# Performance work log

Hardware: AMD Instinct MI355X
Metric: run time of the kernel (lower is better)

The kernel has to match this reference:

```python
import jax, jax.numpy as jnp
import numpy as np

B, S, H, NH = 4, 2048, 1024, 16
HS = H // NH  # head size 64


def setup_inputs() -> dict:
    key = jax.random.key(0)
    ks = jax.random.split(key, 12)
    inv = 1.0 / np.sqrt(H)
    d = {
        "query": jax.random.normal(ks[0], (B, S, H), jnp.float32),
        "key": jax.random.normal(ks[1], (B, S, H), jnp.float32),
        "value": jax.random.normal(ks[2], (B, S, H), jnp.float32),
        "causal_mask": jnp.tril(jnp.ones((S, S), dtype=bool)),
        "Wq": jax.random.uniform(ks[3], (H, H), jnp.float32, -inv, inv),
        "bq": jax.random.uniform(ks[4], (H,), jnp.float32, -inv, inv),
        "Wk": jax.random.uniform(ks[5], (H, H), jnp.float32, -inv, inv),
        "bk": jax.random.uniform(ks[6], (H,), jnp.float32, -inv, inv),
        "Wv": jax.random.uniform(ks[7], (H, H), jnp.float32, -inv, inv),
        "bv": jax.random.uniform(ks[8], (H,), jnp.float32, -inv, inv),
        "Wo": jax.random.uniform(ks[9], (H, H), jnp.float32, -inv, inv),
        "bo": jax.random.uniform(ks[10], (H,), jnp.float32, -inv, inv),
    }
    return d


def reference(query, key, value, causal_mask, Wq, bq, Wk, bk, Wv, bv, Wo, bo):
    # Linear projections (torch Linear: x @ W.T + b)
    q = query @ Wq.T + bq
    k = key @ Wk.T + bk
    v = value @ Wv.T + bv
    # [B, NH, S, HS]
    q = q.reshape(B, S, NH, HS).transpose(0, 2, 1, 3)
    k = k.reshape(B, S, NH, HS).transpose(0, 2, 1, 3)
    v = v.reshape(B, S, NH, HS).transpose(0, 2, 1, 3)
    scores = jnp.einsum("bhqd,bhkd->bhqk", q, k) / jnp.sqrt(jnp.float32(HS))
    scores = jnp.where(causal_mask[None, None, :, :], scores, -jnp.inf)
    attn = jax.nn.softmax(scores, axis=-1)
    ctx = jnp.einsum("bhqk,bhkd->bhqd", attn, v)
    ctx = ctx.transpose(0, 2, 1, 3).reshape(B, S, H)
    return ctx @ Wo.T + bo
```

## Files before the change

### kernel.cpp

```cpp
#include <hip/hip_runtime.h>
#include <hip/hip_bf16.h>
#include <math.h>

#define B_  4
#define S_  2048
#define H_  1024
#define NH_ 16
#define HS_ 64

typedef __attribute__((ext_vector_type(8))) short bf16x8;
typedef __attribute__((ext_vector_type(4))) float f32x4;

__device__ __forceinline__ short f2bf(float f) {
    unsigned u = __builtin_bit_cast(unsigned, f);
    u += 0x7FFFu + ((u >> 16) & 1u);
    return (short)(u >> 16);
}

typedef __attribute__((address_space(3))) void lds_void;
typedef const __attribute__((address_space(1))) void g_void;
__device__ __forceinline__ void gl_lds16(const void* g, void* l) {
    __builtin_amdgcn_global_load_lds((g_void*)g, (lds_void*)l, 16, 0, 0);
}

__global__ __launch_bounds__(256) void cvt_all_k(
    const float* __restrict__ a0, const float* __restrict__ a1,
    const float* __restrict__ a2, const float* __restrict__ w0,
    const float* __restrict__ w1, const float* __restrict__ w2,
    const float* __restrict__ w3,
    short* o0, short* o1, short* o2, short* o3, short* o4, short* o5, short* o6)
{
    const int y = blockIdx.y;
    const float* ins[7]  = {a0, a1, a2, w0, w1, w2, w3};
    short*       outs[7] = {o0, o1, o2, o3, o4, o5, o6};
    const int n8 = (y < 3) ? (int)((size_t)B_ * S_ * H_ / 8) : (int)((size_t)H_ * H_ / 8);
    const int i = blockIdx.x * 256 + threadIdx.x;
    if (i >= n8) return;
    const float4* p = (const float4*)ins[y] + (size_t)i * 2;
    float4 a = p[0], b = p[1];
    bf16x8 o;
    o[0] = f2bf(a.x); o[1] = f2bf(a.y); o[2] = f2bf(a.z); o[3] = f2bf(a.w);
    o[4] = f2bf(b.x); o[5] = f2bf(b.y); o[6] = f2bf(b.z); o[7] = f2bf(b.w);
    *(bf16x8*)(outs[y] + (size_t)i * 8) = o;
}

__device__ __forceinline__ void gemm_core(
    const short* __restrict__ A, const short* __restrict__ W,
    int m0, int n0, short* As, short* Ws, f32x4 acc[4][4])
{
    const int tid  = threadIdx.x;
    const int w    = tid >> 6;
    const int lane = tid & 63;
    const int l15  = lane & 15;
    const int q4   = lane >> 4;
    const int wm   = w >> 1;
    const int wn   = w & 1;
    const int K    = 1024;

    const char* Abase = (const char*)A + (size_t)m0 * K * 2;
    const char* Wbase = (const char*)W + (size_t)n0 * K * 2;

    #pragma unroll
    for (int mi = 0; mi < 4; ++mi)
        #pragma unroll
        for (int ni = 0; ni < 4; ++ni)
            acc[mi][ni] = (f32x4){0.f, 0.f, 0.f, 0.f};

    for (int k0 = 0; k0 < K; k0 += 32) {
        __syncthreads();
        #pragma unroll
        for (int t = 0; t < 2; ++t) {
            const int ob = t * 4096 + w * 1024;
            const int o  = ob + lane * 16;
            const int row = o >> 6;
            const int kb  = o & 63;
            gl_lds16(Abase + (size_t)row * (K * 2) + k0 * 2 + kb, (char*)As + ob);
            gl_lds16(Wbase + (size_t)row * (K * 2) + k0 * 2 + kb, (char*)Ws + ob);
        }
        __syncthreads();

        bf16x8 af[4], bf[4];
        #pragma unroll
        for (int mi = 0; mi < 4; ++mi)
            af[mi] = *(const bf16x8*)(As + (wm * 64 + mi * 16 + l15) * 32 + q4 * 8);
        #pragma unroll
        for (int ni = 0; ni < 4; ++ni)
            bf[ni] = *(const bf16x8*)(Ws + (wn * 64 + ni * 16 + l15) * 32 + q4 * 8);
        #pragma unroll
        for (int mi = 0; mi < 4; ++mi)
            #pragma unroll
            for (int ni = 0; ni < 4; ++ni)
                acc[mi][ni] = __builtin_amdgcn_mfma_f32_16x16x32_bf16(
                    af[mi], bf[ni], acc[mi][ni], 0, 0, 0);
    }
}

__global__ __launch_bounds__(256) void gemm_proj_k(
    const short* __restrict__ Aq, const short* __restrict__ Wqb,
    const float* __restrict__ bq, short* __restrict__ qb,
    const short* __restrict__ Ak, const short* __restrict__ Wkb,
    const float* __restrict__ bk, short* __restrict__ kb,
    const short* __restrict__ Wvb, const short* __restrict__ Av,
    const float* __restrict__ bv, short* __restrict__ vtb)
{
    __shared__ short As[128 * 32];
    __shared__ short Ws[128 * 32];

    const int z = blockIdx.z;
    const short *A, *W; const float* bias; short* out;
    if (z == 0)      { A = Aq;  W = Wqb; bias = bq; out = qb;  }
    else if (z == 1) { A = Ak;  W = Wkb; bias = bk; out = kb;  }
    else             { A = Wvb; W = Av;  bias = bv; out = vtb; }
    const int m0 = (z == 2 ? blockIdx.y : blockIdx.x) * 128;
    const int n0 = (z == 2 ? blockIdx.x : blockIdx.y) * 128;

    f32x4 acc[4][4];
    gemm_core(A, W, m0, n0, As, Ws, acc);

    const int tid  = threadIdx.x;
    const int w    = tid >> 6;
    const int lane = tid & 63;
    const int l15  = lane & 15;
    const int q4   = lane >> 4;
    const int wm   = w >> 1;
    const int wn   = w & 1;

    #pragma unroll
    for (int mi = 0; mi < 4; ++mi) {
        #pragma unroll
        for (int r = 0; r < 4; ++r) {
            const int m = m0 + wm * 64 + mi * 16 + q4 * 4 + r;
            #pragma unroll
            for (int ni = 0; ni < 4; ++ni) {
                const int n = n0 + wn * 64 + ni * 16 + l15;
                const float v = acc[mi][ni][r] + bias[z == 2 ? m : n];
                if (z != 2) {
                    const int b = m >> 11, s = m & (S_ - 1);
                    const int h = n >> 6,  d = n & (HS_ - 1);
                    out[(((size_t)b * NH_ + h) * S_ + s) * HS_ + d] = f2bf(v);
                } else {
                    const int b = n >> 11, s = n & (S_ - 1);
                    const int h = m >> 6,  d = m & (HS_ - 1);
                    out[(((size_t)b * NH_ + h) * HS_ + d) * S_ + s] = f2bf(v);
                }
            }
        }
    }
}

__global__ __launch_bounds__(256) void gemm_out_k(
    const short* __restrict__ A, const short* __restrict__ W,
    const float* __restrict__ bias, float* __restrict__ Cout)
{
    __shared__ short As[128 * 32];
    __shared__ short Ws[128 * 32];
    const int m0 = blockIdx.x * 128;
    const int n0 = blockIdx.y * 128;

    f32x4 acc[4][4];
    gemm_core(A, W, m0, n0, As, Ws, acc);

    const int tid  = threadIdx.x;
    const int w    = tid >> 6;
    const int lane = tid & 63;
    const int l15  = lane & 15;
    const int q4   = lane >> 4;
    const int wm   = w >> 1;
    const int wn   = w & 1;

    #pragma unroll
    for (int mi = 0; mi < 4; ++mi)
        #pragma unroll
        for (int r = 0; r < 4; ++r) {
            const int m = m0 + wm * 64 + mi * 16 + q4 * 4 + r;
            #pragma unroll
            for (int ni = 0; ni < 4; ++ni) {
                const int n = n0 + wn * 64 + ni * 16 + l15;
                Cout[(size_t)m * H_ + n] = acc[mi][ni][r] + bias[n];
            }
        }
}

#define PAD_ 72

__global__ __launch_bounds__(256) void attn_mfma(
    const short* __restrict__ Q, const short* __restrict__ K,
    const short* __restrict__ VT, short* __restrict__ O)
{
    __shared__ short Ks[64 * PAD_];
    __shared__ short Vt[64 * PAD_];
    __shared__ short Pl[4][32 * PAD_];

    const int tid  = threadIdx.x;
    const int w    = tid >> 6;
    const int lane = tid & 63;
    const int l15  = lane & 15;
    const int q4   = lane >> 4;
    const int bh   = blockIdx.y;
    const size_t base = (size_t)bh * S_ * HS_;
    const int b = bh >> 4;
    const int h = bh & 15;
    const float SC = 0.125f * 1.44269504f;

    #pragma unroll 1
    for (int pass = 0; pass < 2; ++pass) {
        const int qt = pass ? (15 - blockIdx.x) : blockIdx.x;

        bf16x8 aQ[2][2];
        #pragma unroll
        for (int mi = 0; mi < 2; ++mi) {
            const int qrow = qt * 128 + w * 32 + mi * 16 + l15;
            #pragma unroll
            for (int kh = 0; kh < 2; ++kh)
                aQ[mi][kh] = *(const bf16x8*)(Q + base + (size_t)qrow * HS_ + kh * 32 + q4 * 8);
        }

        f32x4 accO[2][4];
        float l_p[2][4];
        #pragma unroll
        for (int mi = 0; mi < 2; ++mi) {
            #pragma unroll
            for (int db = 0; db < 4; ++db) accO[mi][db] = (f32x4){0.f, 0.f, 0.f, 0.f};
            #pragma unroll
            for (int r = 0; r < 4; ++r) l_p[mi][r] = 0.f;
        }

        const int ktmax = 2 * qt + 1;
        for (int kt = 0; kt <= ktmax; ++kt) {
            __syncthreads();
            #pragma unroll
            for (int t = 0; t < 2; ++t) {
                const int c  = tid + t * 256;
                const int r  = c >> 3;
                const int e8 = (c & 7) * 8;
                *(bf16x8*)(&Ks[r * PAD_ + e8]) =
                    *(const bf16x8*)(K + base + (size_t)(kt * 64 + r) * HS_ + e8);
                *(bf16x8*)(&Vt[r * PAD_ + e8]) =
                    *(const bf16x8*)(VT + base + (size_t)r * S_ + kt * 64 + e8);
            }
            __syncthreads();

            f32x4 sb[2][4];
            #pragma unroll
            for (int nb = 0; nb < 4; ++nb) {
                const short* kr = &Ks[(nb * 16 + l15) * PAD_ + q4 * 8];
                bf16x8 b0 = *(const bf16x8*)(kr);
                bf16x8 b1 = *(const bf16x8*)(kr + 32);
                #pragma unroll
                for (int mi = 0; mi < 2; ++mi) {
                    f32x4 a = (f32x4){0.f, 0.f, 0.f, 0.f};
                    a = __builtin_amdgcn_mfma_f32_16x16x32_bf16(aQ[mi][0], b0, a, 0, 0, 0);
                    a = __builtin_amdgcn_mfma_f32_16x16x32_bf16(aQ[mi][1], b1, a, 0, 0, 0);
                    sb[mi][nb] = a;
                }
            }

            const bool need_mask = (kt >= 2 * qt);
            #pragma unroll
            for (int mi = 0; mi < 2; ++mi) {
                const int qb0 = qt * 128 + w * 32 + mi * 16 + q4 * 4;
                if (need_mask) {
                    #pragma unroll
                    for (int nb = 0; nb < 4; ++nb) {
                        const int kj = kt * 64 + nb * 16 + l15;
                        #pragma unroll
                        for (int r = 0; r < 4; ++r)
                            if (kj > qb0 + r) sb[mi][nb][r] = -INFINITY;
                    }
                }
                short* pw = &Pl[w][0];
                #pragma unroll
                for (int nb = 0; nb < 4; ++nb) {
                    #pragma unroll
                    for (int r = 0; r < 4; ++r) {
                        const float p = exp2f(sb[mi][nb][r] * SC);
                        l_p[mi][r] += p;
                        pw[(mi * 16 + q4 * 4 + r) * PAD_ + nb * 16 + l15] = f2bf(p);
                    }
                }
            }

            bf16x8 aP[2][2];
            #pragma unroll
            for (int mi = 0; mi < 2; ++mi)
                #pragma unroll
                for (int kh = 0; kh < 2; ++kh)
                    aP[mi][kh] = *(const bf16x8*)(&Pl[w][(mi * 16 + l15) * PAD_ + kh * 32 + q4 * 8]);
            #pragma unroll
            for (int db = 0; db < 4; ++db) {
                const short* vr = &Vt[(db * 16 + l15) * PAD_ + q4 * 8];
                bf16x8 b0 = *(const bf16x8*)(vr);
                bf16x8 b1 = *(const bf16x8*)(vr + 32);
                #pragma unroll
                for (int mi = 0; mi < 2; ++mi) {
                    accO[mi][db] = __builtin_amdgcn_mfma_f32_16x16x32_bf16(aP[mi][0], b0, accO[mi][db], 0, 0, 0);
                    accO[mi][db] = __builtin_amdgcn_mfma_f32_16x16x32_bf16(aP[mi][1], b1, accO[mi][db], 0, 0, 0);
                }
            }
        }

        #pragma unroll
        for (int mi = 0; mi < 2; ++mi) {
            #pragma unroll
            for (int r = 0; r < 4; ++r) {
                float ls = l_p[mi][r];
                ls += __shfl_xor(ls, 1);
                ls += __shfl_xor(ls, 2);
                ls += __shfl_xor(ls, 4);
                ls += __shfl_xor(ls, 8);
                const float inv = 1.f / ls;
                const int orow = qt * 128 + w * 32 + mi * 16 + q4 * 4 + r;
                short* op = O + ((size_t)(b * S_ + orow)) * H_ + h * HS_;
                #pragma unroll
                for (int db = 0; db < 4; ++db)
                    op[db * 16 + l15] = f2bf(accO[mi][db][r] * inv);
            }
        }
        __syncthreads();
    }
}

extern "C" void kernel_launch(void* const* d_in, const int* in_sizes, int n_in,
                              void* d_out, int out_size, void* d_ws, size_t ws_size,
                              hipStream_t stream)
{
    const float* query = (const float*)d_in[0];
    const float* key   = (const float*)d_in[1];
    const float* value = (const float*)d_in[2];
    const float* Wq = (const float*)d_in[4];
    const float* bq = (const float*)d_in[5];
    const float* Wk = (const float*)d_in[6];
    const float* bk = (const float*)d_in[7];
    const float* Wv = (const float*)d_in[8];
    const float* bv = (const float*)d_in[9];
    const float* Wo = (const float*)d_in[10];
    const float* bo = (const float*)d_in[11];
    float* out = (float*)d_out;

    const size_t EA = (size_t)B_ * S_ * H_;
    const size_t EW = (size_t)H_ * H_;

    short* Aq  = (short*)d_ws;
    short* Ak  = Aq  + EA;
    short* Av  = Ak  + EA;
    short* Wqb = Av  + EA;
    short* Wkb = Wqb + EW;
    short* Wvb = Wkb + EW;
    short* Wob = Wvb + EW;
    short* qb  = Wob + EW;
    short* kb  = qb  + EA;
    short* vtb = kb  + EA;
    short* cb  = vtb + EA;

    const int M = B_ * S_;

    cvt_all_k<<<dim3((int)(EA / 8 / 256), 7), 256, 0, stream>>>(
        query, key, value, Wq, Wk, Wv, Wo,
        Aq, Ak, Av, Wqb, Wkb, Wvb, Wob);

    gemm_proj_k<<<dim3(M / 128, H_ / 128, 3), 256, 0, stream>>>(
        Aq, Wqb, bq, qb, Ak, Wkb, bk, kb, Wvb, Av, bv, vtb);

    attn_mfma<<<dim3(S_ / 256, B_ * NH_), 256, 0, stream>>>(qb, kb, vtb, cb);

    gemm_out_k<<<dim3(M / 128, H_ / 128), 256, 0, stream>>>(cb, Wob, bo, out);
}
```

Before: 381.5 us.

## Double GEMM K-tile and load attention K/V tiles via direct global-to-LDS

The projection GEMM core now stages a 64-wide K slice per iteration instead of 32, which halves the number of barrier-separated load phases and runs two MFMA sub-steps per tile. The attention kernel drops its register round-trip for K and V^T tiles and uses global_load_lds directly into unpadded 64-wide LDS rows. The cost is that without padding, LDS reads of K/V rows at a 128-byte stride may hit more bank conflicts, and the GEMM tiles use twice as much shared memory, which can lower occupancy.

```diff
diff --git a/kernel.cpp b/kernel.cpp
--- a/kernel.cpp
+++ b/kernel.cpp
@@ -66,32 +66,35 @@
         for (int ni = 0; ni < 4; ++ni)
             acc[mi][ni] = (f32x4){0.f, 0.f, 0.f, 0.f};
 
-    for (int k0 = 0; k0 < K; k0 += 32) {
+    for (int k0 = 0; k0 < K; k0 += 64) {
         __syncthreads();
         #pragma unroll
-        for (int t = 0; t < 2; ++t) {
+        for (int t = 0; t < 4; ++t) {
             const int ob = t * 4096 + w * 1024;
             const int o  = ob + lane * 16;
-            const int row = o >> 6;
-            const int kb  = o & 63;
+            const int row = o >> 7;
+            const int kb  = o & 127;
             gl_lds16(Abase + (size_t)row * (K * 2) + k0 * 2 + kb, (char*)As + ob);
             gl_lds16(Wbase + (size_t)row * (K * 2) + k0 * 2 + kb, (char*)Ws + ob);
         }
         __syncthreads();
 
-        bf16x8 af[4], bf[4];
-        #pragma unroll
-        for (int mi = 0; mi < 4; ++mi)
-            af[mi] = *(const bf16x8*)(As + (wm * 64 + mi * 16 + l15) * 32 + q4 * 8);
-        #pragma unroll
-        for (int ni = 0; ni < 4; ++ni)
-            bf[ni] = *(const bf16x8*)(Ws + (wn * 64 + ni * 16 + l15) * 32 + q4 * 8);
-        #pragma unroll
-        for (int mi = 0; mi < 4; ++mi)
+        #pragma unroll
+        for (int kh = 0; kh < 2; ++kh) {
+            bf16x8 af[4], bf[4];
+            #pragma unroll
+            for (int mi = 0; mi < 4; ++mi)
+                af[mi] = *(const bf16x8*)(As + (wm * 64 + mi * 16 + l15) * 64 + kh * 32 + q4 * 8);
             #pragma unroll
             for (int ni = 0; ni < 4; ++ni)
-                acc[mi][ni] = __builtin_amdgcn_mfma_f32_16x16x32_bf16(
-                    af[mi], bf[ni], acc[mi][ni], 0, 0, 0);
+                bf[ni] = *(const bf16x8*)(Ws + (wn * 64 + ni * 16 + l15) * 64 + kh * 32 + q4 * 8);
+            #pragma unroll
+            for (int mi = 0; mi < 4; ++mi)
+                #pragma unroll
+                for (int ni = 0; ni < 4; ++ni)
+                    acc[mi][ni] = __builtin_amdgcn_mfma_f32_16x16x32_bf16(
+                        af[mi], bf[ni], acc[mi][ni], 0, 0, 0);
+        }
     }
 }
 
@@ -103,8 +106,8 @@
     const short* __restrict__ Wvb, const short* __restrict__ Av,
     const float* __restrict__ bv, short* __restrict__ vtb)
 {
-    __shared__ short As[128 * 32];
-    __shared__ short Ws[128 * 32];
+    __shared__ short As[128 * 64];
+    __shared__ short Ws[128 * 64];
 
     const int z = blockIdx.z;
     const short *A, *W; const float* bias; short* out;
@@ -152,8 +155,8 @@
     const short* __restrict__ A, const short* __restrict__ W,
     const float* __restrict__ bias, float* __restrict__ Cout)
 {
-    __shared__ short As[128 * 32];
-    __shared__ short Ws[128 * 32];
+    __shared__ short As[128 * 64];
+    __shared__ short Ws[128 * 64];
     const int m0 = blockIdx.x * 128;
     const int n0 = blockIdx.y * 128;
 
@@ -181,15 +184,15 @@
         }
 }
 
-#define PAD_ 72
+#define PPAD_ 72
 
 __global__ __launch_bounds__(256) void attn_mfma(
     const short* __restrict__ Q, const short* __restrict__ K,
     const short* __restrict__ VT, short* __restrict__ O)
 {
-    __shared__ short Ks[64 * PAD_];
-    __shared__ short Vt[64 * PAD_];
-    __shared__ short Pl[4][32 * PAD_];
+    __shared__ short Ks[64 * 64];
+    __shared__ short Vt[64 * 64];
+    __shared__ short Pl[4][32 * PPAD_];
 
     const int tid  = threadIdx.x;
     const int w    = tid >> 6;
@@ -230,20 +233,19 @@
             __syncthreads();
             #pragma unroll
             for (int t = 0; t < 2; ++t) {
-                const int c  = tid + t * 256;
+                const int ob = t * 4096 + w * 1024;
+                const int c  = (ob >> 4) + lane;
                 const int r  = c >> 3;
                 const int e8 = (c & 7) * 8;
-                *(bf16x8*)(&Ks[r * PAD_ + e8]) =
-                    *(const bf16x8*)(K + base + (size_t)(kt * 64 + r) * HS_ + e8);
-                *(bf16x8*)(&Vt[r * PAD_ + e8]) =
-                    *(const bf16x8*)(VT + base + (size_t)r * S_ + kt * 64 + e8);
+                gl_lds16(K + base + (size_t)(kt * 64 + r) * HS_ + e8, (char*)Ks + ob);
+                gl_lds16(VT + base + (size_t)r * S_ + kt * 64 + e8, (char*)Vt + ob);
             }
             __syncthreads();
 
             f32x4 sb[2][4];
             #pragma unroll
             for (int nb = 0; nb < 4; ++nb) {
-                const short* kr = &Ks[(nb * 16 + l15) * PAD_ + q4 * 8];
+                const short* kr = &Ks[(nb * 16 + l15) * 64 + q4 * 8];
                 bf16x8 b0 = *(const bf16x8*)(kr);
                 bf16x8 b1 = *(const bf16x8*)(kr + 32);
                 #pragma unroll
@@ -275,7 +277,7 @@
                     for (int r = 0; r < 4; ++r) {
                         const float p = exp2f(sb[mi][nb][r] * SC);
                         l_p[mi][r] += p;
-                        pw[(mi * 16 + q4 * 4 + r) * PAD_ + nb * 16 + l15] = f2bf(p);
+                        pw[(mi * 16 + q4 * 4 + r) * PPAD_ + nb * 16 + l15] = f2bf(p);
                     }
                 }
             }
@@ -285,10 +287,10 @@
             for (int mi = 0; mi < 2; ++mi)
                 #pragma unroll
                 for (int kh = 0; kh < 2; ++kh)
-                    aP[mi][kh] = *(const bf16x8*)(&Pl[w][(mi * 16 + l15) * PAD_ + kh * 32 + q4 * 8]);
+                    aP[mi][kh] = *(const bf16x8*)(&Pl[w][(mi * 16 + l15) * PPAD_ + kh * 32 + q4 * 8]);
             #pragma unroll
             for (int db = 0; db < 4; ++db) {
-                const short* vr = &Vt[(db * 16 + l15) * PAD_ + q4 * 8];
+                const short* vr = &Vt[(db * 16 + l15) * 64 + q4 * 8];
                 bf16x8 b0 = *(const bf16x8*)(vr);
                 bf16x8 b1 = *(const bf16x8*)(vr + 32);
                 #pragma unroll
```

Result: slower. 399.4 us (+4.7%).
